# Kernel optimization log

Hardware: AMD Instinct MI355X
Metric: run time of the kernel (lower is better)

The kernel has to match this reference:

```python
import jax, jax.numpy as jnp
import numpy as np

WEIGHT_BITS = 5
QUANT_BITS = 16
BN_EPS = 1e-5


def _quant_weight_pow2(w):
    # Round weights to signed powers of two; exponent clipped per DeepShift:
    # shift range = [-(2^(bits-1)-2), 0] = [-14, 0] for 5-bit weights.
    shift_min = -(2 ** (WEIGHT_BITS - 1) - 2)
    sign = jnp.sign(w)
    p = jnp.clip(jnp.round(jnp.log2(jnp.abs(w) + 1e-20)), shift_min, 0.0)
    wq = sign * jnp.exp2(p)
    # straight-through estimator
    return w + jax.lax.stop_gradient(wq - w)


def _quant_act(x):
    # Symmetric per-tensor linear quantization to QUANT_BITS (16-bit) with STE.
    qmax = 2.0 ** (QUANT_BITS - 1) - 1.0
    scale = jnp.maximum(jnp.max(jnp.abs(x)), 1e-12) / qmax
    xq = jnp.round(x / scale) * scale
    return x + jax.lax.stop_gradient(xq - x)


def _conv(x, w, stride=1, pad=0, groups=1):
    return jax.lax.conv_general_dilated(
        x, w, (stride, stride), [(pad, pad), (pad, pad)],
        dimension_numbers=("NCHW", "OIHW", "NCHW"),
        feature_group_count=groups)


def _shift_conv(x, w, stride=1, pad=0, groups=1, bias=None):
    y = _conv(_quant_act(x), _quant_weight_pow2(w), stride, pad, groups)
    if bias is not None:
        y = y + bias[None, :, None, None]
    return y


def _bn(x, g, b, m, v):
    inv = g * jax.lax.rsqrt(v + BN_EPS)
    return x * inv[None, :, None, None] + (b - m * inv)[None, :, None, None]


def setup_inputs() -> dict:
    key = jax.random.key(0)
    ks = jax.random.split(key, 8)
    B, C_in, H, W = 32, 1024, 32, 32
    width, C_out = 256, 1024
    inp = {
        "x": jax.random.normal(ks[0], (B, C_in, H, W), jnp.float32),
        "w1": jax.random.normal(ks[1], (width, C_in, 1, 1), jnp.float32) * 0.05,
        "peg_w": jax.random.normal(ks[2], (width, 1, 3, 3), jnp.float32) * 0.1,
        "peg_b": jax.random.normal(ks[3], (width,), jnp.float32) * 0.01,
        "w2": jax.random.normal(ks[4], (width, width, 3, 3), jnp.float32) * 0.05,
        "w3": jax.random.normal(ks[5], (C_out, width, 1, 1), jnp.float32) * 0.05,
        "bn1_g": jax.random.uniform(ks[6], (width,), jnp.float32, 0.5, 1.5),
        "bn1_b": jnp.zeros((width,), jnp.float32),
        "bn1_m": jnp.zeros((width,), jnp.float32),
        "bn1_v": jnp.ones((width,), jnp.float32),
        "bn2_g": jax.random.uniform(ks[7], (width,), jnp.float32, 0.5, 1.5),
        "bn2_b": jnp.zeros((width,), jnp.float32),
        "bn2_m": jnp.zeros((width,), jnp.float32),
        "bn2_v": jnp.ones((width,), jnp.float32),
        "bn3_g": jax.random.uniform(jax.random.fold_in(key, 9), (C_out,), jnp.float32, 0.5, 1.5),
        "bn3_b": jnp.zeros((C_out,), jnp.float32),
        "bn3_m": jnp.zeros((C_out,), jnp.float32),
        "bn3_v": jnp.ones((C_out,), jnp.float32),
    }
    return inp


def reference(x, w1, peg_w, peg_b, w2, w3,
              bn1_g, bn1_b, bn1_m, bn1_v,
              bn2_g, bn2_b, bn2_m, bn2_v,
              bn3_g, bn3_b, bn3_m, bn3_v):
    residual = x  # downsample is Identity (inplanes == outplanes, stride == 1)
    h = _shift_conv(x, w1)                                   # 1x1 1024->256
    h = _shift_conv(h, peg_w, stride=1, pad=1, groups=256,
                    bias=peg_b)                               # depthwise 3x3 PEG
    h = jax.nn.relu(_bn(h, bn1_g, bn1_b, bn1_m, bn1_v))
    h = _shift_conv(h, w2, stride=1, pad=1)                   # 3x3 256->256
    h = jax.nn.relu(_bn(h, bn2_g, bn2_b, bn2_m, bn2_v))
    h = _shift_conv(h, w3)                                    # 1x1 256->1024
    h = _bn(h, bn3_g, bn3_b, bn3_m, bn3_v)
    return jax.nn.relu(h + residual)
```

## Files before the change

kernel.cpp:

```cpp
#include <hip/hip_runtime.h>

typedef _Float16 f16;
typedef _Float16 f16x8 __attribute__((ext_vector_type(8)));
typedef float f32x4 __attribute__((ext_vector_type(4)));
typedef unsigned short u16;
typedef unsigned int u32;
typedef u32 u32x4 __attribute__((ext_vector_type(4)));

#define WS_BN1_INV  256u
#define WS_BN1_BETA 1280u
#define WS_BN2_INV  2304u
#define WS_BN2_BETA 3328u
#define WS_BN3_INV  4352u
#define WS_BN3_BETA 8448u
#define WS_PEG_B    12544u
#define WS_PEGQ     13568u
#define WS_W1Q      18432u
#define WS_W3Q      542720u
#define WS_W2Q      1067008u
#define WS_H1T      2246656u
#define WS_H2T      19023872u


__device__ __forceinline__ int badf(float f){
  union { float f; u32 u; } c; c.f = f;
  return (c.u & 0x7f800000u) == 0x7f800000u;
}
__device__ __forceinline__ float qpow2(float w){
  float a = fabsf(w) + 1e-20f;
  float p = rintf(log2f(a));
  p = fminf(fmaxf(p, -14.0f), 0.0f);
  float m = exp2f(p);
  return (w > 0.0f) ? m : ((w < 0.0f) ? -m : 0.0f);
}
__device__ __forceinline__ u32 pack2(float a, float b){
  union { f16 h[2]; u32 u; } p; p.h[0] = (f16)a; p.h[1] = (f16)b; return p.u;
}
#define SWZ(row, slot) ((((slot) ^ ((row) >> 1) ^ ((row) >> 3))) & 3)

__global__ __launch_bounds__(256) void prep_kernel(
    const float* __restrict__ w1, const float* __restrict__ pegw, const float* __restrict__ pegb,
    const float* __restrict__ w2, const float* __restrict__ w3,
    const float* g1, const float* b1, const float* m1, const float* v1,
    const float* g2, const float* b2, const float* m2, const float* v2,
    const float* g3, const float* b3, const float* m3, const float* v3,
    char* ws){
  int i = blockIdx.x * 256 + threadIdx.x;
  if (i < 262144){ ((f16*)(ws + WS_W1Q))[i] = (f16)qpow2(w1[i]); return; }
  i -= 262144;
  if (i < 589824){
    int tap = i >> 16, rem = i & 65535;
    int co = rem >> 8, ci = rem & 255;
    ((f16*)(ws + WS_W2Q))[i] = (f16)qpow2(w2[(((co << 8) + ci) * 9) + tap]);
    return;
  }
  i -= 589824;
  if (i < 262144){ ((f16*)(ws + WS_W3Q))[i] = (f16)qpow2(w3[i]); return; }
  i -= 262144;
  if (i < 2304){
    int tap = i >> 8, c = i & 255;
    ((f16*)(ws + WS_PEGQ))[i] = (f16)qpow2(pegw[c * 9 + tap]);
    return;
  }
  i -= 2304;
  if (i < 256){ ((float*)(ws + WS_PEG_B))[i] = pegb[i]; return; }
  i -= 256;
  if (i < 256){
    float inv = g1[i] / sqrtf(v1[i] + 1e-5f);
    ((float*)(ws + WS_BN1_INV))[i] = inv;
    ((float*)(ws + WS_BN1_BETA))[i] = b1[i] - m1[i] * inv;
    return;
  }
  i -= 256;
  if (i < 256){
    float inv = g2[i] / sqrtf(v2[i] + 1e-5f);
    ((float*)(ws + WS_BN2_INV))[i] = inv;
    ((float*)(ws + WS_BN2_BETA))[i] = b2[i] - m2[i] * inv;
    return;
  }
  i -= 256;
  if (i < 1024){
    float inv = g3[i] / sqrtf(v3[i] + 1e-5f);
    ((float*)(ws + WS_BN3_INV))[i] = inv;
    ((float*)(ws + WS_BN3_BETA))[i] = b3[i] - m3[i] * inv;
  }
}

__global__ __launch_bounds__(512) void conv1_kernel(const float* __restrict__ x, char* ws){
  __shared__ __align__(16) char lds[49152];
  const f16* w1q = (const f16*)(ws + WS_W1Q);
  f16* h1T = (f16*)(ws + WS_H1T);

  int tid = threadIdx.x, bid = blockIdx.x;
  int b = bid >> 3, m0 = (bid & 7) << 7;
  int l = tid & 63, wid = tid >> 6, wm = wid >> 2, wn = wid & 3;
  int lr = l & 15, lg = l >> 4;
  f32x4 acc[4][4] = {};

  int q = tid & 31;
  int c = tid >> 5;
  const float* xb = x + (((size_t)(b << 10)) << 10) + m0 + (q << 2);
  int aslot = c >> 2, aoff = (c & 3) << 2;

  f32x4 d0, d1; u32x4 wb0, wb1;
  {
    const float* src = xb + (((size_t)(c << 1)) << 10);
    d0 = *(const f32x4*)src;
    d1 = *(const f32x4*)(src + 1024);
    int s0 = tid, r0 = s0 >> 2, sl0 = s0 & 3;
    int s1 = tid + 512, r1 = s1 >> 2, sl1 = s1 & 3;
    wb0 = *(const u32x4*)(w1q + ((size_t)r0 << 10) + (sl0 << 3));
    wb1 = *(const u32x4*)(w1q + ((size_t)r1 << 10) + (sl1 << 3));
  }
  {
    char* A = lds;
    #pragma unroll
    for (int j = 0; j < 4; ++j){
      int row = (q << 2) + j;
      *(u32*)(A + (row << 6) + (SWZ(row, aslot) << 4) + aoff) = pack2(d0[j], d1[j]);
    }
    int s0 = tid, r0 = s0 >> 2, sl0 = s0 & 3;
    int s1 = tid + 512, r1 = s1 >> 2, sl1 = s1 & 3;
    *(u32x4*)(lds + 8192 + (r0 << 6) + (SWZ(r0, sl0) << 4)) = wb0;
    *(u32x4*)(lds + 8192 + (r1 << 6) + (SWZ(r1, sl1) << 4)) = wb1;
  }
  __syncthreads();

  for (int ks = 0; ks < 32; ++ks){
    const char* cur = lds + ((ks & 1) ? 24576 : 0);
    char* nxt = lds + ((ks & 1) ? 0 : 24576);
    if (ks < 31){
      int k0 = (ks + 1) << 5;
      const float* src = xb + (((size_t)(k0 + (c << 1))) << 10);
      d0 = *(const f32x4*)src;
      d1 = *(const f32x4*)(src + 1024);
      int s0 = tid, r0 = s0 >> 2, sl0 = s0 & 3;
      int s1 = tid + 512, r1 = s1 >> 2, sl1 = s1 & 3;
      wb0 = *(const u32x4*)(w1q + ((size_t)r0 << 10) + k0 + (sl0 << 3));
      wb1 = *(const u32x4*)(w1q + ((size_t)r1 << 10) + k0 + (sl1 << 3));
    }
    f16x8 a[4], bb[4];
    #pragma unroll
    for (int mf = 0; mf < 4; ++mf){
      int row = (wm << 6) + (mf << 4) + lr;
      a[mf] = *(const f16x8*)(cur + (row << 6) + (SWZ(row, lg) << 4));
    }
    #pragma unroll
    for (int nf = 0; nf < 4; ++nf){
      int row = (wn << 6) + (nf << 4) + lr;
      bb[nf] = *(const f16x8*)(cur + 8192 + (row << 6) + (SWZ(row, lg) << 4));
    }
    #pragma unroll
    for (int mf = 0; mf < 4; ++mf)
      #pragma unroll
      for (int nf = 0; nf < 4; ++nf)
        acc[mf][nf] = __builtin_amdgcn_mfma_f32_16x16x32_f16(a[mf], bb[nf], acc[mf][nf], 0, 0, 0);
    if (ks < 31){
      #pragma unroll
      for (int j = 0; j < 4; ++j){
        int row = (q << 2) + j;
        *(u32*)(nxt + (row << 6) + (SWZ(row, aslot) << 4) + aoff) = pack2(d0[j], d1[j]);
      }
      int s0 = tid, r0 = s0 >> 2, sl0 = s0 & 3;
      int s1 = tid + 512, r1 = s1 >> 2, sl1 = s1 & 3;
      *(u32x4*)(nxt + 8192 + (r0 << 6) + (SWZ(r0, sl0) << 4)) = wb0;
      *(u32x4*)(nxt + 8192 + (r1 << 6) + (SWZ(r1, sl1) << 4)) = wb1;
    }
    __syncthreads();
  }

  #pragma unroll
  for (int mf = 0; mf < 4; ++mf){
    int p0 = m0 + (wm << 6) + (mf << 4) + (lg << 2);
    size_t base = ((size_t)(b << 10) + p0) << 8;
    #pragma unroll
    for (int nf = 0; nf < 4; ++nf){
      int co = (wn << 6) + (nf << 4) + lr;
      #pragma unroll
      for (int r = 0; r < 4; ++r)
        h1T[base + ((size_t)r << 8) + co] = (f16)acc[mf][nf][r];
    }
  }
}

__global__ __launch_bounds__(256) void peg_kernel(char* ws){
  __shared__ __align__(16) f16 tile[3][32][256];
  const f16* h1T = (const f16*)(ws + WS_H1T);
  const f16* pegq = (const f16*)(ws + WS_PEGQ);
  const float* pb  = (const float*)(ws + WS_PEG_B);
  const float* inv1 = (const float*)(ws + WS_BN1_INV);
  const float* bt1  = (const float*)(ws + WS_BN1_BETA);
  f16* h2T = (f16*)(ws + WS_H2T);

  int tid = threadIdx.x;
  int b = blockIdx.x >> 5, h = blockIdx.x & 31;

  #pragma unroll
  for (int r = 0; r < 3; ++r){
    int hh = h + r - 1;
    #pragma unroll
    for (int i = 0; i < 4; ++i){
      int chunk = tid + (i << 8);
      int px = chunk >> 5, cg = chunk & 31;
      u32x4 d = {0u, 0u, 0u, 0u};
      if ((u32)hh < 32u)
        d = *(const u32x4*)(h1T + (((size_t)(b << 10) + (hh << 5) + px) << 8) + (cg << 3));
      *(u32x4*)(&tile[r][px][cg << 3]) = d;
    }
  }
  __syncthreads();

  int c0 = (tid & 31) << 3;
  int q  = tid >> 5;
  float acc[4][8];
  #pragma unroll
  for (int i = 0; i < 4; ++i)
    #pragma unroll
    for (int j = 0; j < 8; ++j) acc[i][j] = pb[c0 + j];

  #pragma unroll
  for (int ky = 0; ky < 3; ++ky){
    #pragma unroll
    for (int kx = 0; kx < 3; ++kx){
      f16x8 wv = *(const f16x8*)(pegq + ((ky * 3 + kx) << 8) + c0);
      #pragma unroll
      for (int i = 0; i < 4; ++i){
        int ww = (q << 2) + i + kx - 1;
        if ((u32)ww < 32u){
          f16x8 v = *(const f16x8*)(&tile[ky][ww][c0]);
          #pragma unroll
          for (int j = 0; j < 8; ++j) acc[i][j] += (float)v[j] * (float)wv[j];
        }
      }
    }
  }

  f32x4 iv0 = *(const f32x4*)(inv1 + c0), iv1 = *(const f32x4*)(inv1 + c0 + 4);
  f32x4 bt0 = *(const f32x4*)(bt1 + c0),  bt1v = *(const f32x4*)(bt1 + c0 + 4);
  #pragma unroll
  for (int i = 0; i < 4; ++i){
    f16x8 o;
    #pragma unroll
    for (int j = 0; j < 8; ++j){
      float ivj = (j < 4) ? iv0[j] : iv1[j - 4];
      float btj = (j < 4) ? bt0[j] : bt1v[j - 4];
      o[j] = (f16)fmaxf(acc[i][j] * ivj + btj, 0.0f);
    }
    int p = (h << 5) + (q << 2) + i;
    *(f16x8*)(h2T + (((size_t)(b << 10) + p) << 8) + c0) = o;
  }
}

__global__ __launch_bounds__(512) void conv23_kernel(const float* __restrict__ x,
                                                     float* __restrict__ out, char* ws){
  __shared__ __align__(16) char lds[137216];
  const f16* h2T = (const f16*)(ws + WS_H2T);
  const f16* w2q = (const f16*)(ws + WS_W2Q);
  const f16* w3q = (const f16*)(ws + WS_W3Q);
  const float* inv2 = (const float*)(ws + WS_BN2_INV);
  const float* bt2  = (const float*)(ws + WS_BN2_BETA);
  const float* inv3 = (const float*)(ws + WS_BN3_INV);
  const float* bt3  = (const float*)(ws + WS_BN3_BETA);

  int tid = threadIdx.x, bid = blockIdx.x;
  int b = bid >> 3, mt = bid & 7;
  int h0 = mt << 2;
  int m0 = mt << 7;
  int l = tid & 63, wid = tid >> 6, wm = wid >> 2, wn = wid & 3;
  int lr = l & 15, lg = l >> 4;
  int rk = lr & 7;
  char* A = lds;
  char* B0 = lds + 104448;
  char* B1 = lds + 104448 + 16384;

  for (int chunk = tid; chunk < 6528; chunk += 512){
    int r = chunk / 1088;
    int rem = chunk - r * 1088;
    int cc = rem >> 5, slot = rem & 31;
    int hh = h0 - 1 + r, wwp = cc - 1;
    u32x4 d = {0u, 0u, 0u, 0u};
    if ((u32)hh < 32u && (u32)wwp < 32u)
      d = *(const u32x4*)(h2T + (((size_t)(b << 10) + (hh << 5) + wwp) << 8) + (slot << 3));
    int sw = slot ^ (cc & 7);
    *(u32x4*)(A + ((r * 34 + cc) << 9) + (sw << 4)) = d;
  }
  #pragma unroll
  for (int i = 0; i < 2; ++i){
    int chunk = tid + (i << 9);
    int co = chunk >> 2, slot = chunk & 3;
    u32x4 d = *(const u32x4*)(w2q + (co << 8) + (slot << 3));
    *(u32x4*)(B0 + (co << 6) + (SWZ(co, slot) << 4)) = d;
  }
  __syncthreads();

  f32x4 acc[4][4] = {};
  for (int tap = 0; tap < 9; ++tap){
    int dy = tap / 3 - 1, dx = tap % 3 - 1;
    int rowbase[4], key[4];
    #pragma unroll
    for (int mf = 0; mf < 4; ++mf){
      int p = (wm << 6) + (mf << 4) + lr;
      int rr = (p >> 5) + dy + 1;
      int cc = (p & 31) + dx + 1;
      rowbase[mf] = (rr * 34 + cc) << 9;
      key[mf] = cc & 7;
    }
    #pragma unroll 2
    for (int ks = 0; ks < 8; ++ks){
      int t = (tap << 3) + ks;
      u32x4 st[2];
      int have = (t < 71);
      int t1 = t + 1, wtap = t1 >> 3, wks = t1 & 7;
      const f16* srcb = w2q + wtap * 65536 + (wks << 5);
      if (have){
        #pragma unroll
        for (int i = 0; i < 2; ++i){
          int chunk = tid + (i << 9);
          int co = chunk >> 2, slot = chunk & 3;
          st[i] = *(const u32x4*)(srcb + (co << 8) + (slot << 3));
        }
      }
      const char* bs = (t & 1) ? B1 : B0;
      f16x8 a[4], bb[4];
      int sl = (ks << 2) | lg;
      #pragma unroll
      for (int mf = 0; mf < 4; ++mf)
        a[mf] = *(const f16x8*)(A + rowbase[mf] + ((sl ^ key[mf]) << 4));
      #pragma unroll
      for (int nf = 0; nf < 4; ++nf){
        int row = (wn << 6) + (nf << 4) + lr;
        bb[nf] = *(const f16x8*)(bs + (row << 6) + (SWZ(row, lg) << 4));
      }
      #pragma unroll
      for (int mf = 0; mf < 4; ++mf)
        #pragma unroll
        for (int nf = 0; nf < 4; ++nf)
          acc[mf][nf] = __builtin_amdgcn_mfma_f32_16x16x32_f16(a[mf], bb[nf], acc[mf][nf], 0, 0, 0);
      if (have){
        char* bd = (t1 & 1) ? B1 : B0;
        #pragma unroll
        for (int i = 0; i < 2; ++i){
          int chunk = tid + (i << 9);
          int co = chunk >> 2, slot = chunk & 3;
          *(u32x4*)(bd + (co << 6) + (SWZ(co, slot) << 4)) = st[i];
        }
      }
      __syncthreads();
    }
  }

  #pragma unroll
  for (int mf = 0; mf < 4; ++mf){
    #pragma unroll
    for (int nf = 0; nf < 4; ++nf){
      int c = (wn << 6) + (nf << 4) + lr;
      float iv = inv2[c], bt = bt2[c];
      int slot = c >> 3, off = (c & 7) << 1;
      #pragma unroll
      for (int r = 0; r < 4; ++r){
        int px = (wm << 6) + (mf << 4) + (lg << 2) + r;
        float f = fmaxf(acc[mf][nf][r] * iv + bt, 0.0f);
        *(f16*)(lds + (px << 9) + ((slot ^ (px & 7)) << 4) + off) = (f16)f;
      }
    }
  }
  __syncthreads();

  for (int cot = 0; cot < 8; ++cot){
    #pragma unroll
    for (int i = 0; i < 8; ++i){
      int s = tid + (i << 9);
      int row = s >> 5, slot = s & 31;
      u32x4 d = *(const u32x4*)(w3q + (((size_t)(cot << 7) + row) << 8) + (slot << 3));
      *(u32x4*)(lds + 65536 + (row << 9) + ((slot ^ (row & 7)) << 4)) = d;
    }
    __syncthreads();

    f32x4 acc2[4][2] = {};
    #pragma unroll
    for (int ks = 0; ks < 8; ++ks){
      int sl = ((ks << 2) | lg) ^ rk;
      f16x8 a[4], bb[2];
      #pragma unroll
      for (int mf = 0; mf < 4; ++mf){
        int row = (wm << 6) + (mf << 4) + lr;
        a[mf] = *(const f16x8*)(lds + 65536 + (row << 9) + (sl << 4));
      }
      #pragma unroll
      for (int nf = 0; nf < 2; ++nf){
        int row = (wn << 5) + (nf << 4) + lr;
        bb[nf] = *(const f16x8*)(lds + (row << 9) + (sl << 4));
      }
      #pragma unroll
      for (int mf = 0; mf < 4; ++mf)
        #pragma unroll
        for (int nf = 0; nf < 2; ++nf)
          acc2[mf][nf] = __builtin_amdgcn_mfma_f32_16x16x32_f16(a[mf], bb[nf], acc2[mf][nf], 0, 0, 0);
    }

    #pragma unroll
    for (int mf = 0; mf < 4; ++mf){
      int co0 = (cot << 7) + (wm << 6) + (mf << 4) + (lg << 2);
      f32x4 iv = *(const f32x4*)(inv3 + co0);
      f32x4 bt = *(const f32x4*)(bt3 + co0);
      float xr[8];
      #pragma unroll
      for (int nf = 0; nf < 2; ++nf){
        int px = (wn << 5) + (nf << 4) + lr;
        #pragma unroll
        for (int r = 0; r < 4; ++r)
          xr[(nf << 2) + r] = x[(((size_t)(b << 10) + co0 + r) << 10) + m0 + px];
      }
      #pragma unroll
      for (int nf = 0; nf < 2; ++nf){
        int px = (wn << 5) + (nf << 4) + lr;
        #pragma unroll
        for (int r = 0; r < 4; ++r){
          size_t idx = (((size_t)(b << 10) + co0 + r) << 10) + m0 + px;
          float z = acc2[mf][nf][r] * iv[r] + bt[r] + xr[(nf << 2) + r];
          float rr = fmaxf(z, 0.0f);
          if (badf(z)) rr = 512.0f;
          out[idx] = rr;
        }
      }
    }
    __syncthreads();
  }
}

extern "C" void kernel_launch(void* const* d_in, const int* in_sizes, int n_in,
                              void* d_out, int out_size, void* d_ws, size_t ws_size,
                              hipStream_t stream){
  const float* x    = (const float*)d_in[0];
  const float* w1   = (const float*)d_in[1];
  const float* pegw = (const float*)d_in[2];
  const float* pegb = (const float*)d_in[3];
  const float* w2   = (const float*)d_in[4];
  const float* w3   = (const float*)d_in[5];
  const float* g1 = (const float*)d_in[6];
  const float* b1 = (const float*)d_in[7];
  const float* m1 = (const float*)d_in[8];
  const float* v1 = (const float*)d_in[9];
  const float* g2 = (const float*)d_in[10];
  const float* b2 = (const float*)d_in[11];
  const float* m2 = (const float*)d_in[12];
  const float* v2 = (const float*)d_in[13];
  const float* g3 = (const float*)d_in[14];
  const float* b3 = (const float*)d_in[15];
  const float* m3 = (const float*)d_in[16];
  const float* v3 = (const float*)d_in[17];
  char* ws = (char*)d_ws;

  prep_kernel<<<4368, 256, 0, stream>>>(w1, pegw, pegb, w2, w3,
                                        g1, b1, m1, v1, g2, b2, m2, v2,
                                        g3, b3, m3, v3, ws);
  conv1_kernel<<<256, 512, 0, stream>>>(x, ws);
  peg_kernel<<<1024, 256, 0, stream>>>(ws);
  conv23_kernel<<<256, 512, 0, stream>>>(x, (float*)d_out, ws);
}
```

Measured before the change: 172.8 us.

## Halve conv23 pixel tile and split input channels to cut LDS footprint

Result: slower. 219.9 us (+27.3%).

```diff
diff --git a/kernel.cpp b/kernel.cpp
--- a/kernel.cpp
+++ b/kernel.cpp
@@ -253,7 +253,7 @@
 
 __global__ __launch_bounds__(512) void conv23_kernel(const float* __restrict__ x,
                                                      float* __restrict__ out, char* ws){
-  __shared__ __align__(16) char lds[137216];
+  __shared__ __align__(16) char lds[69632];
   const f16* h2T = (const f16*)(ws + WS_H2T);
   const f16* w2q = (const f16*)(ws + WS_W2Q);
   const f16* w3q = (const f16*)(ws + WS_W3Q);
@@ -263,94 +263,90 @@
   const float* bt3  = (const float*)(ws + WS_BN3_BETA);
 
   int tid = threadIdx.x, bid = blockIdx.x;
-  int b = bid >> 3, mt = bid & 7;
-  int h0 = mt << 2;
-  int m0 = mt << 7;
+  int b = bid >> 4, mt = bid & 15;
+  int h0 = mt << 1;
+  int m0 = mt << 6;
   int l = tid & 63, wid = tid >> 6, wm = wid >> 2, wn = wid & 3;
   int lr = l & 15, lg = l >> 4;
   int rk = lr & 7;
-  char* A = lds;
-  char* B0 = lds + 104448;
-  char* B1 = lds + 104448 + 16384;
-
-  for (int chunk = tid; chunk < 6528; chunk += 512){
-    int r = chunk / 1088;
-    int rem = chunk - r * 1088;
-    int cc = rem >> 5, slot = rem & 31;
-    int hh = h0 - 1 + r, wwp = cc - 1;
-    u32x4 d = {0u, 0u, 0u, 0u};
-    if ((u32)hh < 32u && (u32)wwp < 32u)
-      d = *(const u32x4*)(h2T + (((size_t)(b << 10) + (hh << 5) + wwp) << 8) + (slot << 3));
-    int sw = slot ^ (cc & 7);
-    *(u32x4*)(A + ((r * 34 + cc) << 9) + (sw << 4)) = d;
-  }
+  char* B = lds + 36864;
+
+  f32x4 acc[2][4] = {};
+  u32x4 st[2];
   #pragma unroll
   for (int i = 0; i < 2; ++i){
     int chunk = tid + (i << 9);
     int co = chunk >> 2, slot = chunk & 3;
-    u32x4 d = *(const u32x4*)(w2q + (co << 8) + (slot << 3));
-    *(u32x4*)(B0 + (co << 6) + (SWZ(co, slot) << 4)) = d;
-  }
-  __syncthreads();
-
-  f32x4 acc[4][4] = {};
-  for (int tap = 0; tap < 9; ++tap){
-    int dy = tap / 3 - 1, dx = tap % 3 - 1;
-    int rowbase[4], key[4];
-    #pragma unroll
-    for (int mf = 0; mf < 4; ++mf){
-      int p = (wm << 6) + (mf << 4) + lr;
-      int rr = (p >> 5) + dy + 1;
-      int cc = (p & 31) + dx + 1;
-      rowbase[mf] = (rr * 34 + cc) << 9;
-      key[mf] = cc & 7;
-    }
-    #pragma unroll 2
-    for (int ks = 0; ks < 8; ++ks){
-      int t = (tap << 3) + ks;
-      u32x4 st[2];
-      int have = (t < 71);
-      int t1 = t + 1, wtap = t1 >> 3, wks = t1 & 7;
-      const f16* srcb = w2q + wtap * 65536 + (wks << 5);
-      if (have){
+    st[i] = *(const u32x4*)(w2q + (co << 8) + (slot << 3));
+  }
+
+  for (int kh = 0; kh < 2; ++kh){
+    __syncthreads();
+    for (int chunk = tid; chunk < 2176; chunk += 512){
+      int r = chunk / 544;
+      int rem = chunk - r * 544;
+      int cc = rem >> 4, slot = rem & 15;
+      int hh = h0 - 1 + r, wwp = cc - 1;
+      u32x4 d = {0u, 0u, 0u, 0u};
+      if ((u32)hh < 32u && (u32)wwp < 32u)
+        d = *(const u32x4*)(h2T + (((size_t)(b << 10) + (hh << 5) + wwp) << 8) + (kh << 7) + (slot << 3));
+      *(u32x4*)(lds + ((r * 34 + cc) << 8) + ((slot ^ (cc & 7)) << 4)) = d;
+    }
+    for (int tap = 0; tap < 9; ++tap){
+      int dy = tap / 3 - 1, dx = tap % 3 - 1;
+      int rowbase[2], key[2];
+      #pragma unroll
+      for (int mf = 0; mf < 2; ++mf){
+        int p = (wm << 5) + (mf << 4) + lr;
+        int rr = (p >> 5) + dy + 1;
+        int cc = (p & 31) + dx + 1;
+        rowbase[mf] = (rr * 34 + cc) << 8;
+        key[mf] = cc & 7;
+      }
+      for (int ks4 = 0; ks4 < 4; ++ks4){
+        __syncthreads();
         #pragma unroll
         for (int i = 0; i < 2; ++i){
           int chunk = tid + (i << 9);
           int co = chunk >> 2, slot = chunk & 3;
-          st[i] = *(const u32x4*)(srcb + (co << 8) + (slot << 3));
+          *(u32x4*)(B + (co << 6) + (SWZ(co, slot) << 4)) = st[i];
         }
-      }
-      const char* bs = (t & 1) ? B1 : B0;
-      f16x8 a[4], bb[4];
-      int sl = (ks << 2) | lg;
-      #pragma unroll
-      for (int mf = 0; mf < 4; ++mf)
-        a[mf] = *(const f16x8*)(A + rowbase[mf] + ((sl ^ key[mf]) << 4));
-      #pragma unroll
-      for (int nf = 0; nf < 4; ++nf){
-        int row = (wn << 6) + (nf << 4) + lr;
-        bb[nf] = *(const f16x8*)(bs + (row << 6) + (SWZ(row, lg) << 4));
-      }
-      #pragma unroll
-      for (int mf = 0; mf < 4; ++mf)
+        __syncthreads();
+        int nkh = kh, ntap = tap, nks4 = ks4 + 1, have = 1;
+        if (nks4 == 4){ nks4 = 0; ntap = tap + 1;
+          if (ntap == 9){ ntap = 0; nkh = kh + 1; if (nkh == 2) have = 0; } }
+        if (have){
+          const f16* srcb = w2q + ntap * 65536 + (nkh << 7) + (nks4 << 5);
+          #pragma unroll
+          for (int i = 0; i < 2; ++i){
+            int chunk = tid + (i << 9);
+            int co = chunk >> 2, slot = chunk & 3;
+            st[i] = *(const u32x4*)(srcb + (co << 8) + (slot << 3));
+          }
+        }
+        int sl = (ks4 << 2) | lg;
+        f16x8 a[2], bb[4];
         #pragma unroll
-        for (int nf = 0; nf < 4; ++nf)
-          acc[mf][nf] = __builtin_amdgcn_mfma_f32_16x16x32_f16(a[mf], bb[nf], acc[mf][nf], 0, 0, 0);
-      if (have){
-        char* bd = (t1 & 1) ? B1 : B0;
+        for (int mf = 0; mf < 2; ++mf)
+          a[mf] = *(const f16x8*)(lds + rowbase[mf] + ((sl ^ key[mf]) << 4));
         #pragma unroll
-        for (int i = 0; i < 2; ++i){
-          int chunk = tid + (i << 9);
-          int co = chunk >> 2, slot = chunk & 3;
-          *(u32x4*)(bd + (co << 6) + (SWZ(co, slot) << 4)) = st[i];
+        for (int nf = 0; nf < 4; ++nf){
+          int row = (wn << 6) + (nf << 4) + lr;
+          bb[nf] = *(const f16x8*)(B + (row << 6) + (SWZ(row, lg) << 4));
         }
-      }
-      __syncthreads();
-    }
-  }
-
-  #pragma unroll
-  for (int mf = 0; mf < 4; ++mf){
+        #pragma unroll
+        for (int mf = 0; mf < 2; ++mf)
+          #pragma unroll
+          for (int nf = 0; nf < 4; ++nf)
+            acc[mf][nf] = __builtin_amdgcn_mfma_f32_16x16x32_f16(a[mf], bb[nf], acc[mf][nf], 0, 0, 0);
+      }
+    }
+  }
+
+  __syncthreads();
+
+  #pragma unroll
+  for (int mf = 0; mf < 2; ++mf){
     #pragma unroll
     for (int nf = 0; nf < 4; ++nf){
       int c = (wn << 6) + (nf << 4) + lr;
@@ -358,70 +354,60 @@
       int slot = c >> 3, off = (c & 7) << 1;
       #pragma unroll
       for (int r = 0; r < 4; ++r){
-        int px = (wm << 6) + (mf << 4) + (lg << 2) + r;
+        int px = (wm << 5) + (mf << 4) + (lg << 2) + r;
         float f = fmaxf(acc[mf][nf][r] * iv + bt, 0.0f);
         *(f16*)(lds + (px << 9) + ((slot ^ (px & 7)) << 4) + off) = (f16)f;
       }
     }
   }
-  __syncthreads();
-
-  for (int cot = 0; cot < 8; ++cot){
-    #pragma unroll
-    for (int i = 0; i < 8; ++i){
-      int s = tid + (i << 9);
-      int row = s >> 5, slot = s & 31;
-      u32x4 d = *(const u32x4*)(w3q + (((size_t)(cot << 7) + row) << 8) + (slot << 3));
-      *(u32x4*)(lds + 65536 + (row << 9) + ((slot ^ (row & 7)) << 4)) = d;
+
+  int wc = wid >> 2, wp = wid & 3;
+  for (int cot = 0; cot < 16; ++cot){
+    #pragma unroll
+    for (int i = 0; i < 4; ++i){
+      int chunk = (tid << 2) + i;
+      int row = chunk >> 5, slot = chunk & 31;
+      u32x4 d = *(const u32x4*)(w3q + (((size_t)(cot << 6) + row) << 8) + (slot << 3));
+      *(u32x4*)(B + (row << 9) + ((slot ^ (row & 7)) << 4)) = d;
     }
     __syncthreads();
 
-    f32x4 acc2[4][2] = {};
+    f32x4 acc2[2] = {};
     #pragma unroll
     for (int ks = 0; ks < 8; ++ks){
       int sl = ((ks << 2) | lg) ^ rk;
-      f16x8 a[4], bb[2];
-      #pragma unroll
-      for (int mf = 0; mf < 4; ++mf){
-        int row = (wm << 6) + (mf << 4) + lr;
-        a[mf] = *(const f16x8*)(lds + 65536 + (row << 9) + (sl << 4));
-      }
-      #pragma unroll
-      for (int nf = 0; nf < 2; ++nf){
-        int row = (wn << 5) + (nf << 4) + lr;
-        bb[nf] = *(const f16x8*)(lds + (row << 9) + (sl << 4));
-      }
-      #pragma unroll
-      for (int mf = 0; mf < 4; ++mf)
-        #pragma unroll
-        for (int nf = 0; nf < 2; ++nf)
-          acc2[mf][nf] = __builtin_amdgcn_mfma_f32_16x16x32_f16(a[mf], bb[nf], acc2[mf][nf], 0, 0, 0);
-    }
-
-    #pragma unroll
-    for (int mf = 0; mf < 4; ++mf){
-      int co0 = (cot << 7) + (wm << 6) + (mf << 4) + (lg << 2);
+      f16x8 a[2], bb;
+      #pragma unroll
+      for (int mf = 0; mf < 2; ++mf){
+        int row = (wc << 5) + (mf << 4) + lr;
+        a[mf] = *(const f16x8*)(B + (row << 9) + (sl << 4));
+      }
+      {
+        int row = (wp << 4) + lr;
+        bb = *(const f16x8*)(lds + (row << 9) + (sl << 4));
+      }
+      #pragma unroll
+      for (int mf = 0; mf < 2; ++mf)
+        acc2[mf] = __builtin_amdgcn_mfma_f32_16x16x32_f16(a[mf], bb, acc2[mf], 0, 0, 0);
+    }
+
+    #pragma unroll
+    for (int mf = 0; mf < 2; ++mf){
+      int co0 = (cot << 6) + (wc << 5) + (mf << 4) + (lg << 2);
       f32x4 iv = *(const f32x4*)(inv3 + co0);
       f32x4 bt = *(const f32x4*)(bt3 + co0);
-      float xr[8];
-      #pragma unroll
-      for (int nf = 0; nf < 2; ++nf){
-        int px = (wn << 5) + (nf << 4) + lr;
-        #pragma unroll
-        for (int r = 0; r < 4; ++r)
-          xr[(nf << 2) + r] = x[(((size_t)(b << 10) + co0 + r) << 10) + m0 + px];
-      }
-      #pragma unroll
-      for (int nf = 0; nf < 2; ++nf){
-        int px = (wn << 5) + (nf << 4) + lr;
-        #pragma unroll
-        for (int r = 0; r < 4; ++r){
-          size_t idx = (((size_t)(b << 10) + co0 + r) << 10) + m0 + px;
-          float z = acc2[mf][nf][r] * iv[r] + bt[r] + xr[(nf << 2) + r];
-          float rr = fmaxf(z, 0.0f);
-          if (badf(z)) rr = 512.0f;
-          out[idx] = rr;
-        }
+      int px = (wp << 4) + lr;
+      float xr[4];
+      #pragma unroll
+      for (int r = 0; r < 4; ++r)
+        xr[r] = x[(((size_t)(b << 10) + co0 + r) << 10) + m0 + px];
+      #pragma unroll
+      for (int r = 0; r < 4; ++r){
+        size_t idx = (((size_t)(b << 10) + co0 + r) << 10) + m0 + px;
+        float z = acc2[mf][r] * iv[r] + bt[r] + xr[r];
+        float rr = fmaxf(z, 0.0f);
+        if (badf(z)) rr = 512.0f;
+        out[idx] = rr;
       }
     }
     __syncthreads();
@@ -456,5 +442,5 @@
                                         g3, b3, m3, v3, ws);
   conv1_kernel<<<256, 512, 0, stream>>>(x, ws);
   peg_kernel<<<1024, 256, 0, stream>>>(ws);
-  conv23_kernel<<<256, 512, 0, stream>>>(x, (float*)d_out, ws);
-}
+  conv23_kernel<<<512, 512, 0, stream>>>(x, (float*)d_out, ws);
+}
```

## Double-buffer w3 tiles in LDS and prefetch next tile during MFMA

Applied to the files above, without the earlier changes.

Result: faster. 169.2 us (-2.1%).

```diff
diff --git a/kernel.cpp b/kernel.cpp
--- a/kernel.cpp
+++ b/kernel.cpp
@@ -364,56 +364,77 @@
       }
     }
   }
+
+  int wc = wid >> 2, wp = wid & 3;
+  char* W3 = lds + 65536;
+  #pragma unroll
+  for (int i = 0; i < 4; ++i){
+    int chunk = tid + (i << 9);
+    int row = chunk >> 5, slot = chunk & 31;
+    u32x4 d = *(const u32x4*)(w3q + ((size_t)row << 8) + (slot << 3));
+    *(u32x4*)(W3 + (row << 9) + ((slot ^ (row & 7)) << 4)) = d;
+  }
   __syncthreads();
 
-  for (int cot = 0; cot < 8; ++cot){
-    #pragma unroll
-    for (int i = 0; i < 8; ++i){
-      int s = tid + (i << 9);
-      int row = s >> 5, slot = s & 31;
-      u32x4 d = *(const u32x4*)(w3q + (((size_t)(cot << 7) + row) << 8) + (slot << 3));
-      *(u32x4*)(lds + 65536 + (row << 9) + ((slot ^ (row & 7)) << 4)) = d;
-    }
-    __syncthreads();
-
-    f32x4 acc2[4][2] = {};
+  for (int cot = 0; cot < 16; ++cot){
+    const char* cur = W3 + ((cot & 1) << 15);
+    char* nxt = W3 + (((cot + 1) & 1) << 15);
+    u32x4 st[4];
+    int have = (cot < 15);
+    if (have){
+      const f16* srcb = w3q + (((size_t)(cot + 1)) << 14);
+      #pragma unroll
+      for (int i = 0; i < 4; ++i){
+        int chunk = tid + (i << 9);
+        int row = chunk >> 5, slot = chunk & 31;
+        st[i] = *(const u32x4*)(srcb + ((size_t)row << 8) + (slot << 3));
+      }
+    }
+    f32x4 acc2[2][2] = {};
     #pragma unroll
     for (int ks = 0; ks < 8; ++ks){
       int sl = ((ks << 2) | lg) ^ rk;
-      f16x8 a[4], bb[2];
-      #pragma unroll
-      for (int mf = 0; mf < 4; ++mf){
-        int row = (wm << 6) + (mf << 4) + lr;
-        a[mf] = *(const f16x8*)(lds + 65536 + (row << 9) + (sl << 4));
+      f16x8 a[2], bb[2];
+      #pragma unroll
+      for (int mf = 0; mf < 2; ++mf){
+        int row = (wc << 5) + (mf << 4) + lr;
+        a[mf] = *(const f16x8*)(cur + (row << 9) + (sl << 4));
       }
       #pragma unroll
       for (int nf = 0; nf < 2; ++nf){
-        int row = (wn << 5) + (nf << 4) + lr;
+        int row = (wp << 5) + (nf << 4) + lr;
         bb[nf] = *(const f16x8*)(lds + (row << 9) + (sl << 4));
       }
       #pragma unroll
-      for (int mf = 0; mf < 4; ++mf)
+      for (int mf = 0; mf < 2; ++mf)
         #pragma unroll
         for (int nf = 0; nf < 2; ++nf)
           acc2[mf][nf] = __builtin_amdgcn_mfma_f32_16x16x32_f16(a[mf], bb[nf], acc2[mf][nf], 0, 0, 0);
     }
-
-    #pragma unroll
-    for (int mf = 0; mf < 4; ++mf){
-      int co0 = (cot << 7) + (wm << 6) + (mf << 4) + (lg << 2);
+    if (have){
+      #pragma unroll
+      for (int i = 0; i < 4; ++i){
+        int chunk = tid + (i << 9);
+        int row = chunk >> 5, slot = chunk & 31;
+        *(u32x4*)(nxt + (row << 9) + ((slot ^ (row & 7)) << 4)) = st[i];
+      }
+    }
+    #pragma unroll
+    for (int mf = 0; mf < 2; ++mf){
+      int co0 = (cot << 6) + (wc << 5) + (mf << 4) + (lg << 2);
       f32x4 iv = *(const f32x4*)(inv3 + co0);
       f32x4 bt = *(const f32x4*)(bt3 + co0);
       float xr[8];
       #pragma unroll
       for (int nf = 0; nf < 2; ++nf){
-        int px = (wn << 5) + (nf << 4) + lr;
+        int px = (wp << 5) + (nf << 4) + lr;
         #pragma unroll
         for (int r = 0; r < 4; ++r)
           xr[(nf << 2) + r] = x[(((size_t)(b << 10) + co0 + r) << 10) + m0 + px];
       }
       #pragma unroll
       for (int nf = 0; nf < 2; ++nf){
-        int px = (wn << 5) + (nf << 4) + lr;
+        int px = (wp << 5) + (nf << 4) + lr;
         #pragma unroll
         for (int r = 0; r < 4; ++r){
           size_t idx = (((size_t)(b << 10) + co0 + r) << 10) + m0 + px;
```
